# Optimization experiments

Measured on AMD Instinct MI355X. Metric: run time of the kernel, lower is better.

## Reference

```python
import jax, jax.numpy as jnp
import numpy as np

N_SAMPLES, N_NODES, IN_CH, HID, OUT_CH = 262144, 24, 32, 32, 1

def setup_inputs() -> dict:
    key = jax.random.key(0)
    k = jax.random.split(key, 6)
    h = jax.random.normal(k[0], (N_SAMPLES, N_NODES, IN_CH), dtype=jnp.float32)
    valid = jax.random.randint(k[1], (N_SAMPLES, N_NODES), 0, 2, dtype=jnp.int32)
    # per-node MLP params, PyTorch-style init scale ~ 1/sqrt(fan_in)
    W1 = jax.random.normal(k[2], (N_NODES, IN_CH, HID), dtype=jnp.float32) / np.sqrt(IN_CH)
    b1 = jax.random.normal(k[3], (N_NODES, HID), dtype=jnp.float32) / np.sqrt(IN_CH)
    W2 = jax.random.normal(k[4], (N_NODES, HID, OUT_CH), dtype=jnp.float32) / np.sqrt(HID)
    b2 = jax.random.normal(k[5], (N_NODES, OUT_CH), dtype=jnp.float32) / np.sqrt(HID)
    return {"h": h, "valid": valid, "W1": W1, "b1": b1, "W2": W2, "b2": b2}

def reference(h, valid, W1, b1, W2, b2):
    # Per-node MLP: input ReLU -> Linear(in,W) -> ReLU -> Linear(W,out).
    # Instead of a Python loop with gather/scatter over nodes, run all
    # nodes as a batched (grouped) GEMM and mask invalid entries to zero
    # (the torch code leaves invalid slots at their zero init).
    x = jax.nn.relu(h)                                    # [S, N, C]
    x = jax.nn.relu(jnp.einsum('snc,ncw->snw', x, W1) + b1[None])  # [S, N, W]
    out = jnp.einsum('snw,nwo->sno', x, W2) + b2[None]    # [S, N, O]
    mask = (valid > 0)[:, :, None]                        # [S, N, 1]
    return jnp.where(mask, out, jnp.zeros((), out.dtype))
```

## Files before the change

kernel.cpp:

```cpp
#include <hip/hip_runtime.h>

#define NS 262144
#define NN 24
#define CI 32
#define HW 32

typedef _Float16 half8 __attribute__((ext_vector_type(8)));
typedef float f32x4 __attribute__((ext_vector_type(4)));
typedef unsigned int u32x4 __attribute__((ext_vector_type(4)));

__device__ alignas(16) unsigned short g_w1f[NN * 2 * 64 * 8];

__global__ void pack_w1(const float* __restrict__ W1) {
  int idx = blockIdx.x * 256 + threadIdx.x;
  if (idx >= NN * 2 * 64 * 8) return;
  int i    = idx & 7;
  int lane = (idx >> 3) & 63;
  int hf   = (idx >> 9) & 1;
  int n    = idx >> 10;
  int k = (lane >> 4) * 8 + i;
  int w = hf * 16 + (lane & 15);
  _Float16 v = (_Float16)W1[(n * CI + k) * HW + w];
  g_w1f[idx] = __builtin_bit_cast(unsigned short, v);
}

__global__ __launch_bounds__(256) void mlp_mfma(
    const float* __restrict__ h, const int* __restrict__ valid,
    const float* __restrict__ b1, const float* __restrict__ W2,
    const float* __restrict__ b2, float* __restrict__ out) {
  const int tid  = threadIdx.x;
  const int lane = tid & 63;
  const int wv   = tid >> 6;
  const int r    = lane & 15;
  const int q    = lane >> 4;
  const int sB   = blockIdx.x * 256;

  for (int n = 0; n < NN; ++n) {
    half8 Af0 = __builtin_bit_cast(half8,
        *(const u32x4*)&g_w1f[((n * 2 + 0) * 64 + lane) * 8]);
    half8 Af1 = __builtin_bit_cast(half8,
        *(const u32x4*)&g_w1f[((n * 2 + 1) * 64 + lane) * 8]);
    f32x4 b1a = *(const f32x4*)&b1[n * HW + q * 4];
    f32x4 b1b = *(const f32x4*)&b1[n * HW + 16 + q * 4];
    f32x4 w2a = *(const f32x4*)&W2[n * HW + q * 4];
    f32x4 w2b = *(const f32x4*)&W2[n * HW + 16 + q * 4];
    float b2n = b2[n];

#pragma unroll
    for (int t = 0; t < 4; ++t) {
      const int s0   = sB + wv * 64 + t * 16;
      const int srow = s0 + r;

      const int vld = valid[srow * NN + n];
      f32x4 av0 = {0.f, 0.f, 0.f, 0.f}, av1 = {0.f, 0.f, 0.f, 0.f};
      if (vld) {
        const float* hp = &h[((size_t)srow * NN + n) * CI + q * 8];
        av0 = *(const f32x4*)hp;
        av1 = *(const f32x4*)(hp + 4);
      }

      half8 Hf;
      Hf[0] = (_Float16)fmaxf(av0[0], 0.f);
      Hf[1] = (_Float16)fmaxf(av0[1], 0.f);
      Hf[2] = (_Float16)fmaxf(av0[2], 0.f);
      Hf[3] = (_Float16)fmaxf(av0[3], 0.f);
      Hf[4] = (_Float16)fmaxf(av1[0], 0.f);
      Hf[5] = (_Float16)fmaxf(av1[1], 0.f);
      Hf[6] = (_Float16)fmaxf(av1[2], 0.f);
      Hf[7] = (_Float16)fmaxf(av1[3], 0.f);

      f32x4 c0 = {b1a[0], b1a[1], b1a[2], b1a[3]};
      f32x4 c1 = {b1b[0], b1b[1], b1b[2], b1b[3]};
      c0 = __builtin_amdgcn_mfma_f32_16x16x32_f16(Af0, Hf, c0, 0, 0, 0);
      c1 = __builtin_amdgcn_mfma_f32_16x16x32_f16(Af1, Hf, c1, 0, 0, 0);

      float p = 0.f;
#pragma unroll
      for (int i = 0; i < 4; ++i) {
        p = fmaf(fmaxf(c0[i], 0.f), w2a[i], p);
        p = fmaf(fmaxf(c1[i], 0.f), w2b[i], p);
      }
      p += __shfl_xor(p, 16);
      p += __shfl_xor(p, 32);

      if (lane < 16)
        out[(size_t)srow * NN + n] = vld ? (p + b2n) : 0.0f;
    }
  }
}

extern "C" void kernel_launch(void* const* d_in, const int* in_sizes, int n_in,
                              void* d_out, int out_size, void* d_ws, size_t ws_size,
                              hipStream_t stream) {
  const float* h     = (const float*)d_in[0];
  const int*   valid = (const int*)d_in[1];
  const float* W1    = (const float*)d_in[2];
  const float* b1    = (const float*)d_in[3];
  const float* W2    = (const float*)d_in[4];
  const float* b2    = (const float*)d_in[5];
  float* out = (float*)d_out;

  hipLaunchKernelGGL(pack_w1, dim3((NN * 2 * 64 * 8 + 255) / 256), dim3(256),
                     0, stream, W1);
  hipLaunchKernelGGL(mlp_mfma, dim3(NS / 256), dim3(256), 0, stream,
                     h, valid, b1, W2, b2, out);
}
```

Measured before the change: 231.0 us.

## Software-pipeline node loop with prefetched h/valid loads and packed fp16 conversion

Restructures the per-node loop so the h loads for node n+1 and the valid flags for node n+2 are issued before the MFMA work for node n. This hides global memory latency behind compute. It also converts to fp16 with a packed round-toward-zero instruction instead of per-element casts, and adds a min-blocks occupancy hint of 4. The cost is extra live registers, and the conversion now rounds toward zero rather than to nearest.

```diff
diff --git a/kernel.cpp b/kernel.cpp
--- a/kernel.cpp
+++ b/kernel.cpp
@@ -5,6 +5,8 @@
 #define CI 32
 #define HW 32
 
+typedef _Float16 half2v __attribute__((ext_vector_type(2)));
+typedef __fp16 fp16x2v __attribute__((ext_vector_type(2)));
 typedef _Float16 half8 __attribute__((ext_vector_type(8)));
 typedef float f32x4 __attribute__((ext_vector_type(4)));
 typedef unsigned int u32x4 __attribute__((ext_vector_type(4)));
@@ -24,7 +26,19 @@
   g_w1f[idx] = __builtin_bit_cast(unsigned short, v);
 }
 
-__global__ __launch_bounds__(256) void mlp_mfma(
+__device__ __forceinline__ unsigned pkrtz(float a, float b) {
+#if __has_builtin(__builtin_amdgcn_cvt_pkrtz)
+  fp16x2v p = __builtin_amdgcn_cvt_pkrtz(a, b);
+  return __builtin_bit_cast(unsigned, p);
+#else
+  half2v p;
+  p[0] = (_Float16)a;
+  p[1] = (_Float16)b;
+  return __builtin_bit_cast(unsigned, p);
+#endif
+}
+
+__global__ __launch_bounds__(256, 4) void mlp_mfma(
     const float* __restrict__ h, const int* __restrict__ valid,
     const float* __restrict__ b1, const float* __restrict__ W2,
     const float* __restrict__ b2, float* __restrict__ out) {
@@ -34,6 +48,29 @@
   const int r    = lane & 15;
   const int q    = lane >> 4;
   const int sB   = blockIdx.x * 256;
+
+  int srow[4];
+#pragma unroll
+  for (int t = 0; t < 4; ++t) srow[t] = sB + wv * 64 + t * 16 + r;
+
+  int vcur[4], vnext[4], vfut[4];
+#pragma unroll
+  for (int t = 0; t < 4; ++t) {
+    vcur[t]  = valid[srow[t] * NN + 0];
+    vnext[t] = valid[srow[t] * NN + 1];
+  }
+
+  f32x4 raw0[4], raw1[4];
+#pragma unroll
+  for (int t = 0; t < 4; ++t) {
+    raw0[t] = (f32x4){0.f, 0.f, 0.f, 0.f};
+    raw1[t] = (f32x4){0.f, 0.f, 0.f, 0.f};
+    if (vcur[t]) {
+      const float* hp = &h[(size_t)(srow[t] * NN) * CI + q * 8];
+      raw0[t] = *(const f32x4*)hp;
+      raw1[t] = *(const f32x4*)(hp + 4);
+    }
+  }
 
   for (int n = 0; n < NN; ++n) {
     half8 Af0 = __builtin_bit_cast(half8,
@@ -46,33 +83,35 @@
     f32x4 w2b = *(const f32x4*)&W2[n * HW + 16 + q * 4];
     float b2n = b2[n];
 
+    half8 Hf[4];
 #pragma unroll
     for (int t = 0; t < 4; ++t) {
-      const int s0   = sB + wv * 64 + t * 16;
-      const int srow = s0 + r;
+      unsigned u0 = pkrtz(fmaxf(raw0[t][0], 0.f), fmaxf(raw0[t][1], 0.f));
+      unsigned u1 = pkrtz(fmaxf(raw0[t][2], 0.f), fmaxf(raw0[t][3], 0.f));
+      unsigned u2 = pkrtz(fmaxf(raw1[t][0], 0.f), fmaxf(raw1[t][1], 0.f));
+      unsigned u3 = pkrtz(fmaxf(raw1[t][2], 0.f), fmaxf(raw1[t][3], 0.f));
+      u32x4 uu = {u0, u1, u2, u3};
+      Hf[t] = __builtin_bit_cast(half8, uu);
+    }
 
-      const int vld = valid[srow * NN + n];
-      f32x4 av0 = {0.f, 0.f, 0.f, 0.f}, av1 = {0.f, 0.f, 0.f, 0.f};
-      if (vld) {
-        const float* hp = &h[((size_t)srow * NN + n) * CI + q * 8];
-        av0 = *(const f32x4*)hp;
-        av1 = *(const f32x4*)(hp + 4);
+    const int nn1 = (n + 1 < NN) ? n + 1 : NN - 1;
+    const int nn2 = (n + 2 < NN) ? n + 2 : NN - 1;
+#pragma unroll
+    for (int t = 0; t < 4; ++t) {
+      vfut[t] = valid[srow[t] * NN + nn2];
+      if (vnext[t]) {
+        const float* hp = &h[(size_t)(srow[t] * NN + nn1) * CI + q * 8];
+        raw0[t] = *(const f32x4*)hp;
+        raw1[t] = *(const f32x4*)(hp + 4);
       }
+    }
 
-      half8 Hf;
-      Hf[0] = (_Float16)fmaxf(av0[0], 0.f);
-      Hf[1] = (_Float16)fmaxf(av0[1], 0.f);
-      Hf[2] = (_Float16)fmaxf(av0[2], 0.f);
-      Hf[3] = (_Float16)fmaxf(av0[3], 0.f);
-      Hf[4] = (_Float16)fmaxf(av1[0], 0.f);
-      Hf[5] = (_Float16)fmaxf(av1[1], 0.f);
-      Hf[6] = (_Float16)fmaxf(av1[2], 0.f);
-      Hf[7] = (_Float16)fmaxf(av1[3], 0.f);
-
+#pragma unroll
+    for (int t = 0; t < 4; ++t) {
       f32x4 c0 = {b1a[0], b1a[1], b1a[2], b1a[3]};
       f32x4 c1 = {b1b[0], b1b[1], b1b[2], b1b[3]};
-      c0 = __builtin_amdgcn_mfma_f32_16x16x32_f16(Af0, Hf, c0, 0, 0, 0);
-      c1 = __builtin_amdgcn_mfma_f32_16x16x32_f16(Af1, Hf, c1, 0, 0, 0);
+      c0 = __builtin_amdgcn_mfma_f32_16x16x32_f16(Af0, Hf[t], c0, 0, 0, 0);
+      c1 = __builtin_amdgcn_mfma_f32_16x16x32_f16(Af1, Hf[t], c1, 0, 0, 0);
 
       float p = 0.f;
 #pragma unroll
@@ -84,7 +123,13 @@
       p += __shfl_xor(p, 32);
 
       if (lane < 16)
-        out[(size_t)srow * NN + n] = vld ? (p + b2n) : 0.0f;
+        out[(size_t)srow[t] * NN + n] = vcur[t] ? (p + b2n) : 0.0f;
+    }
+
+#pragma unroll
+    for (int t = 0; t < 4; ++t) {
+      vcur[t]  = vnext[t];
+      vnext[t] = vfut[t];
     }
   }
 }
```

Result: no change. 229.0 us (-0.9%).

## Stage h tile through LDS with coalesced loads and per-wave node split

Applied to the files above, without the earlier changes.

Each block now covers 32 samples instead of 256. It loads the block's contiguous h slice with fully coalesced 16-byte reads, applies ReLU, packs to fp16 with pkrtz, and stores it to LDS using an XOR swizzle. Each wave then handles 6 of the 24 nodes and reads its MFMA B operands from LDS. This replaces the strided per-node global reads (a 128-byte chunk every 3 KB), so DRAM access should become sequential. The cost is an LDS round trip, a block-wide barrier, and reloading the W1 fragments more often because there are 8x more blocks.

```diff
diff --git a/kernel.cpp b/kernel.cpp
--- a/kernel.cpp
+++ b/kernel.cpp
@@ -1,13 +1,19 @@
 #include <hip/hip_runtime.h>
 
-#define NS 262144
-#define NN 24
-#define CI 32
-#define HW 32
+#define NS  262144
+#define NN  24
+#define CI  32
+#define HW  32
+#define SPB 32
+#define NROWS (SPB * NN)
+#define NCHUNK (NROWS * 8)
 
+typedef __fp16 fp16x2v __attribute__((ext_vector_type(2)));
+typedef _Float16 half2v __attribute__((ext_vector_type(2)));
 typedef _Float16 half8 __attribute__((ext_vector_type(8)));
 typedef float f32x4 __attribute__((ext_vector_type(4)));
 typedef unsigned int u32x4 __attribute__((ext_vector_type(4)));
+typedef unsigned int u32x2 __attribute__((ext_vector_type(2)));
 
 __device__ alignas(16) unsigned short g_w1f[NN * 2 * 64 * 8];
 
@@ -24,18 +30,54 @@
   g_w1f[idx] = __builtin_bit_cast(unsigned short, v);
 }
 
+__device__ __forceinline__ unsigned pkrtz(float a, float b) {
+#if __has_builtin(__builtin_amdgcn_cvt_pkrtz)
+  fp16x2v p = __builtin_amdgcn_cvt_pkrtz(a, b);
+  return __builtin_bit_cast(unsigned, p);
+#else
+  half2v p;
+  p[0] = (_Float16)a;
+  p[1] = (_Float16)b;
+  return __builtin_bit_cast(unsigned, p);
+#endif
+}
+
 __global__ __launch_bounds__(256) void mlp_mfma(
     const float* __restrict__ h, const int* __restrict__ valid,
     const float* __restrict__ b1, const float* __restrict__ W2,
     const float* __restrict__ b2, float* __restrict__ out) {
-  const int tid  = threadIdx.x;
+  __shared__ alignas(16) unsigned short lds[NN * SPB * CI];
+
+  const int tid = threadIdx.x;
+  const int sB  = blockIdx.x * SPB;
+  const float* __restrict__ gb = h + (size_t)sB * (NN * CI);
+  const int*   __restrict__ vb = valid + sB * NN;
+
+#pragma unroll 8
+  for (int rd = 0; rd < NCHUNK / 256; ++rd) {
+    const int chunk = rd * 256 + tid;
+    const int rloc  = chunk >> 3;
+    const int c0    = (chunk & 7) * 4;
+    const int v     = vb[rloc];
+    f32x4 d = {0.f, 0.f, 0.f, 0.f};
+    if (v) d = *(const f32x4*)(gb + (size_t)chunk * 4);
+    const int sl = rloc / NN;
+    const int n  = rloc - sl * NN;
+    unsigned p0 = pkrtz(fmaxf(d[0], 0.f), fmaxf(d[1], 0.f));
+    unsigned p1 = pkrtz(fmaxf(d[2], 0.f), fmaxf(d[3], 0.f));
+    int byte = n * (SPB * CI * 2) + sl * (CI * 2) + c0 * 2;
+    byte ^= (n & 7) << 6;
+    *(u32x2*)((char*)lds + byte) = (u32x2){p0, p1};
+  }
+  __syncthreads();
+
   const int lane = tid & 63;
   const int wv   = tid >> 6;
   const int r    = lane & 15;
   const int q    = lane >> 4;
-  const int sB   = blockIdx.x * 256;
 
-  for (int n = 0; n < NN; ++n) {
+  for (int ni = 0; ni < 6; ++ni) {
+    const int n = wv * 6 + ni;
     half8 Af0 = __builtin_bit_cast(half8,
         *(const u32x4*)&g_w1f[((n * 2 + 0) * 64 + lane) * 8]);
     half8 Af1 = __builtin_bit_cast(half8,
@@ -47,27 +89,10 @@
     float b2n = b2[n];
 
 #pragma unroll
-    for (int t = 0; t < 4; ++t) {
-      const int s0   = sB + wv * 64 + t * 16;
-      const int srow = s0 + r;
-
-      const int vld = valid[srow * NN + n];
-      f32x4 av0 = {0.f, 0.f, 0.f, 0.f}, av1 = {0.f, 0.f, 0.f, 0.f};
-      if (vld) {
-        const float* hp = &h[((size_t)srow * NN + n) * CI + q * 8];
-        av0 = *(const f32x4*)hp;
-        av1 = *(const f32x4*)(hp + 4);
-      }
-
-      half8 Hf;
-      Hf[0] = (_Float16)fmaxf(av0[0], 0.f);
-      Hf[1] = (_Float16)fmaxf(av0[1], 0.f);
-      Hf[2] = (_Float16)fmaxf(av0[2], 0.f);
-      Hf[3] = (_Float16)fmaxf(av0[3], 0.f);
-      Hf[4] = (_Float16)fmaxf(av1[0], 0.f);
-      Hf[5] = (_Float16)fmaxf(av1[1], 0.f);
-      Hf[6] = (_Float16)fmaxf(av1[2], 0.f);
-      Hf[7] = (_Float16)fmaxf(av1[3], 0.f);
+    for (int sh = 0; sh < 2; ++sh) {
+      int byte = n * (SPB * CI * 2) + (sh * 16 + r) * (CI * 2) + q * 16;
+      byte ^= (n & 7) << 6;
+      half8 Hf = *(const half8*)((const char*)lds + byte);
 
       f32x4 c0 = {b1a[0], b1a[1], b1a[2], b1a[3]};
       f32x4 c1 = {b1b[0], b1b[1], b1b[2], b1b[3]};
@@ -83,8 +108,11 @@
       p += __shfl_xor(p, 16);
       p += __shfl_xor(p, 32);
 
-      if (lane < 16)
-        out[(size_t)srow * NN + n] = vld ? (p + b2n) : 0.0f;
+      if (lane < 16) {
+        const int srow = sB + sh * 16 + r;
+        const int vv = valid[srow * NN + n];
+        out[(size_t)srow * NN + n] = vv ? (p + b2n) : 0.0f;
+      }
     }
   }
 }
@@ -102,6 +130,6 @@
 
   hipLaunchKernelGGL(pack_w1, dim3((NN * 2 * 64 * 8 + 255) / 256), dim3(256),
                      0, stream, W1);
-  hipLaunchKernelGGL(mlp_mfma, dim3(NS / 256), dim3(256), 0, stream,
+  hipLaunchKernelGGL(mlp_mfma, dim3(NS / SPB), dim3(256), 0, stream,
                      h, valid, b1, W2, b2, out);
 }
```

Result: slower. 282.5 us (+22.3%).
